# Kernel optimization log

Hardware: AMD Instinct MI355X
Metric: run time of the kernel (lower is better)

Reference implementation:

```python
import jax, jax.numpy as jnp
import numpy as np

D_MODEL = 1024
N_HEADS = 16
D_K = D_MODEL // N_HEADS
B, S = 2, 2048


def setup_inputs() -> dict:
    key = jax.random.key(0)
    ks = jax.random.split(key, 12)
    s = 1.0 / np.sqrt(D_MODEL)
    inp = {
        "query": jax.random.normal(ks[0], (B, S, D_MODEL), jnp.float32),
        "key": jax.random.normal(ks[1], (B, S, D_MODEL), jnp.float32),
        "value": jax.random.normal(ks[2], (B, S, D_MODEL), jnp.float32),
        "W_q": jax.random.uniform(ks[3], (D_MODEL, D_MODEL), jnp.float32, -s, s),
        "b_q": jnp.zeros((D_MODEL,), jnp.float32),
        "W_k": jax.random.uniform(ks[4], (D_MODEL, D_MODEL), jnp.float32, -s, s),
        "b_k": jnp.zeros((D_MODEL,), jnp.float32),
        "W_v": jax.random.uniform(ks[5], (D_MODEL, D_MODEL), jnp.float32, -s, s),
        "b_v": jnp.zeros((D_MODEL,), jnp.float32),
        "W_o": jax.random.uniform(ks[6], (D_MODEL, D_MODEL), jnp.float32, -s, s),
        "b_o": jnp.zeros((D_MODEL,), jnp.float32),
        "ln_gamma": jnp.ones((D_MODEL,), jnp.float32),
        "ln_beta": jnp.zeros((D_MODEL,), jnp.float32),
    }
    return inp


def _layer_norm(x, gamma, beta, eps=1e-5):
    mu = jnp.mean(x, axis=-1, keepdims=True)
    var = jnp.var(x, axis=-1, keepdims=True)
    return (x - mu) * jax.lax.rsqrt(var + eps) * gamma + beta


def reference(query, key, value, W_q, b_q, W_k, b_k, W_v, b_v, W_o, b_o, ln_gamma, ln_beta):
    b, s, _ = query.shape
    # projections -> [b, h, s, d_k]
    q = (query @ W_q.T + b_q).reshape(b, s, N_HEADS, D_K).transpose(0, 2, 1, 3)
    k = (key @ W_k.T + b_k).reshape(b, s, N_HEADS, D_K).transpose(0, 2, 1, 3)
    v = (value @ W_v.T + b_v).reshape(b, s, N_HEADS, D_K).transpose(0, 2, 1, 3)
    # scaled dot-product attention (no mask)
    scores = jnp.einsum('bhqd,bhkd->bhqk', q, k) / jnp.sqrt(jnp.float32(D_K))
    attn = jax.nn.softmax(scores, axis=-1)
    ctx = jnp.einsum('bhqk,bhkd->bhqd', attn, v)  # [b,h,s,d_k]
    ctx = ctx.transpose(0, 2, 1, 3).reshape(b, s, D_MODEL)
    out = ctx @ W_o.T + b_o
    # residual uses the PROJECTED query (quirk of original module); dropout=identity (eval)
    resid = q.transpose(0, 2, 1, 3).reshape(b, s, D_MODEL)
    return _layer_norm(out + resid, ln_gamma, ln_beta)
```

## Files before the change

### kernel.cpp

```cpp
#include <hip/hip_runtime.h>

#define DM 1024
#define NH 16
#define DKq 64
#define BB 2
#define SS 2048
#define MTOT 4096

#define K2f 0.18033688011112042f
#define IK2f 5.545177444479562f

typedef __attribute__((ext_vector_type(4))) float f32x4;
typedef __attribute__((ext_vector_type(16))) float f32x16;
typedef __attribute__((ext_vector_type(8))) short s16x8;
typedef __attribute__((ext_vector_type(4))) short s16x4;
typedef __attribute__((ext_vector_type(4))) unsigned short u16x4;

__device__ __forceinline__ unsigned short f2bf(float f) {
    unsigned u = __float_as_uint(f);
    u += 0x7fff + ((u >> 16) & 1);
    return (unsigned short)(u >> 16);
}

__device__ __forceinline__ float bf2f(unsigned short x) {
    return __uint_as_float((unsigned)x << 16);
}

__device__ __forceinline__ s16x8 cvt8(f32x4 a, f32x4 b) {
    s16x8 r;
    r[0] = (short)f2bf(a[0]); r[1] = (short)f2bf(a[1]);
    r[2] = (short)f2bf(a[2]); r[3] = (short)f2bf(a[3]);
    r[4] = (short)f2bf(b[0]); r[5] = (short)f2bf(b[1]);
    r[6] = (short)f2bf(b[2]); r[7] = (short)f2bf(b[3]);
    return r;
}

__device__ __forceinline__ unsigned pkp(float a, float b) {
    return __builtin_amdgcn_perm(__float_as_uint(b), __float_as_uint(a), 0x07060302u);
}

__device__ __forceinline__ void gload_lds16(const void* g, void* l) {
    __builtin_amdgcn_global_load_lds(
        (const __attribute__((address_space(1))) unsigned int*)g,
        (__attribute__((address_space(3))) unsigned int*)l,
        16, 0, 0);
}

__global__ __launch_bounds__(256)
void cvt_kernel(const float* __restrict__ s0, const float* __restrict__ s1,
                const float* __restrict__ s2, const float* __restrict__ s3,
                const float* __restrict__ s4, const float* __restrict__ s5,
                const float* __restrict__ s6,
                unsigned short* __restrict__ Xb, unsigned short* __restrict__ Wb)
{
    const int seg = blockIdx.y;
    const float* src;
    unsigned short* dst;
    int n;
    if (seg < 3) {
        src = (seg == 0) ? s0 : (seg == 1) ? s1 : s2;
        dst = Xb + (size_t)seg * (MTOT * DM);
        n = MTOT * DM;
    } else {
        src = (seg == 3) ? s3 : (seg == 4) ? s4 : (seg == 5) ? s5 : s6;
        dst = Wb + (size_t)(seg - 3) * (DM * DM);
        n = DM * DM;
    }
    const int stride = gridDim.x * 256;
    for (int i = blockIdx.x * 256 + threadIdx.x; i * 8 < n; i += stride) {
        f32x4 a = *(const f32x4*)(src + (size_t)i * 8);
        f32x4 b = *(const f32x4*)(src + (size_t)i * 8 + 4);
        *(s16x8*)(dst + (size_t)i * 8) = cvt8(a, b);
    }
}

__global__ __launch_bounds__(256, 3)
void proj_kernel(const unsigned short* __restrict__ Xb,
                 const unsigned short* __restrict__ Wb,
                 const float* __restrict__ bq, const float* __restrict__ bk,
                 const float* __restrict__ bv,
                 unsigned short* __restrict__ Qh, unsigned short* __restrict__ Kh,
                 unsigned short* __restrict__ Vt)
{
    const int bid = blockIdx.x;
    const int t   = (bid & 7) * 96 + (bid >> 3);
    const int z   = t >> 8;
    const int ty  = (t >> 3) & 31;
    const int tx  = t & 7;

    const unsigned short* X = Xb + (size_t)z * (MTOT * DM);
    const unsigned short* W = Wb + (size_t)z * (DM * DM);
    const float* bias = (z == 0) ? bq : (z == 1) ? bk : bv;

    const int m0 = ty * 128;
    const int n0 = tx * 128;
    const int tid  = threadIdx.x;
    const int lane = tid & 63;
    const int w    = tid >> 6;
    const int wm   = w >> 1, wn = w & 1;

    __shared__ __align__(16) short lA[2][128 * 32];
    __shared__ __align__(16) short lB[2][128 * 32];

    f32x4 acc[4][4];
#pragma unroll
    for (int i = 0; i < 4; i++)
#pragma unroll
        for (int j = 0; j < 4; j++) acc[i][j] = (f32x4)(0.f);

    const int srow16 = lane >> 2;
    const int scg    = lane & 3;

#define PSTAGE(BUF, KC) {                                                     \
    const int k0_ = (KC) * 32;                                                \
    _Pragma("unroll")                                                         \
    for (int p = 0; p < 2; ++p) {                                             \
        int c = w * 2 + p;                                                    \
        int row = c * 16 + srow16;                                            \
        int kc = scg ^ ((row >> 1) & 3);                                      \
        gload_lds16(X + (size_t)(m0 + row) * DM + k0_ + kc * 8,               \
                    (char*)lA[BUF] + c * 1024);                               \
        gload_lds16(W + (size_t)(n0 + row) * DM + k0_ + kc * 8,               \
                    (char*)lB[BUF] + c * 1024);                               \
    } }

#define PCOMPUTE(BUF) {                                                       \
    s16x8 af[4], bf[4];                                                       \
    const int kq = lane >> 4;                                                 \
    _Pragma("unroll")                                                         \
    for (int i = 0; i < 4; i++) {                                             \
        int row = wm * 64 + i * 16 + (lane & 15);                             \
        int slot = kq ^ ((row >> 1) & 3);                                     \
        af[i] = *(const s16x8*)((const char*)lA[BUF] + row * 64 + slot * 16); \
    }                                                                         \
    _Pragma("unroll")                                                         \
    for (int i = 0; i < 4; i++) {                                             \
        int row = wn * 64 + i * 16 + (lane & 15);                             \
        int slot = kq ^ ((row >> 1) & 3);                                     \
        bf[i] = *(const s16x8*)((const char*)lB[BUF] + row * 64 + slot * 16); \
    }                                                                         \
    _Pragma("unroll")                                                         \
    for (int i = 0; i < 4; i++)                                               \
        _Pragma("unroll")                                                     \
        for (int j = 0; j < 4; j++)                                           \
            acc[i][j] = __builtin_amdgcn_mfma_f32_16x16x32_bf16(              \
                af[i], bf[j], acc[i][j], 0, 0, 0);                            \
    }

    PSTAGE(0, 0);
    __syncthreads();
    for (int kp = 0; kp < 16; ++kp) {
        const int k2 = kp * 2;
        if (k2 + 1 < 32) PSTAGE(1, k2 + 1);
        PCOMPUTE(0);
        __syncthreads();
        if (k2 + 2 < 32) PSTAGE(0, k2 + 2);
        PCOMPUTE(1);
        __syncthreads();
    }
#undef PSTAGE
#undef PCOMPUTE

#pragma unroll
    for (int i = 0; i < 4; i++) {
#pragma unroll
        for (int j = 0; j < 4; j++) {
            int rg0 = m0 + wm * 64 + i * 16 + 4 * (lane >> 4);
            int cg  = n0 + wn * 64 + j * 16 + (lane & 15);
            int b = rg0 >> 11, s0 = rg0 & 2047, h = cg >> 6, d = cg & 63;
            float bv_ = bias[cg];
            if (z == 2) {
                int s0p = (s0 & ~12) | ((s0 & 4) << 1) | ((s0 & 8) >> 1);
                u16x4 st;
#pragma unroll
                for (int e = 0; e < 4; e++) st[e] = f2bf(acc[i][j][e] + bv_);
                *(u16x4*)&Vt[(((size_t)(b * NH + h)) * DKq + d) * SS + s0p] = st;
            } else if (z == 0) {
#pragma unroll
                for (int e = 0; e < 4; e++)
                    Qh[(((size_t)(b * NH + h)) * SS + s0 + e) * DKq + d] =
                        f2bf((acc[i][j][e] + bv_) * K2f);
            } else {
#pragma unroll
                for (int e = 0; e < 4; e++)
                    Kh[(((size_t)(b * NH + h)) * SS + s0 + e) * DKq + d] =
                        f2bf(acc[i][j][e] + bv_);
            }
        }
    }
}

__device__ __forceinline__ void attn_tile32(
    const char* __restrict__ lkc, const char* __restrict__ lvc,
    const s16x8* aq, s16x8 onesv, int l31, int hi,
    f32x16& o0, f32x16& o1, f32x16& o4)
{
    f32x16 s0 = (f32x16)(0.f), s1 = (f32x16)(0.f);
    const int sw = (l31 & 7) << 4;
    __builtin_amdgcn_s_setprio(1);
#pragma unroll
    for (int kkd = 0; kkd < 4; kkd++) {
        const int byte = (32 * kkd + 16 * hi) ^ sw;
        s16x8 ak0 = *(const s16x8*)(lkc + l31 * 128 + byte);
        s0 = __builtin_amdgcn_mfma_f32_32x32x16_bf16(ak0, aq[kkd], s0, 0, 0, 0);
        s16x8 ak1 = *(const s16x8*)(lkc + (32 + l31) * 128 + byte);
        s1 = __builtin_amdgcn_mfma_f32_32x32x16_bf16(ak1, aq[kkd], s1, 0, 0, 0);
    }
    __builtin_amdgcn_s_setprio(0);

#pragma unroll
    for (int r = 0; r < 16; r++) {
        s0[r] = __builtin_amdgcn_exp2f(s0[r]);
        s1[r] = __builtin_amdgcn_exp2f(s1[r]);
    }

    __builtin_amdgcn_s_setprio(1);
#pragma unroll
    for (int jb = 0; jb < 2; jb++) {
#pragma unroll
        for (int u = 0; u < 2; u++) {
            const int t = 2 * jb + u;
            union { unsigned uu[4]; s16x8 v; } bp;
            if (jb == 0) {
                bp.uu[0] = pkp(s0[8*u+0], s0[8*u+1]);
                bp.uu[1] = pkp(s0[8*u+2], s0[8*u+3]);
                bp.uu[2] = pkp(s0[8*u+4], s0[8*u+5]);
                bp.uu[3] = pkp(s0[8*u+6], s0[8*u+7]);
            } else {
                bp.uu[0] = pkp(s1[8*u+0], s1[8*u+1]);
                bp.uu[1] = pkp(s1[8*u+2], s1[8*u+3]);
                bp.uu[2] = pkp(s1[8*u+4], s1[8*u+5]);
                bp.uu[3] = pkp(s1[8*u+6], s1[8*u+7]);
            }
            const int vbyte = (32 * t + 16 * hi) ^ sw;
            s16x8 av0 = *(const s16x8*)(lvc + l31 * 128 + vbyte);
            o0 = __builtin_amdgcn_mfma_f32_32x32x16_bf16(av0, bp.v, o0, 0, 0, 0);
            s16x8 av1 = *(const s16x8*)(lvc + (32 + l31) * 128 + vbyte);
            o1 = __builtin_amdgcn_mfma_f32_32x32x16_bf16(av1, bp.v, o1, 0, 0, 0);
            o4 = __builtin_amdgcn_mfma_f32_32x32x16_bf16(onesv, bp.v, o4, 0, 0, 0);
        }
    }
    __builtin_amdgcn_s_setprio(0);
}

__global__ __launch_bounds__(256)
void attn_kernel(const unsigned short* __restrict__ Qh,
                 const unsigned short* __restrict__ Kh,
                 const unsigned short* __restrict__ Vt,
                 unsigned short* __restrict__ Ctx)
{
    const int bid = blockIdx.x;
    const int tt  = (bid & 7) * 64 + (bid >> 3);
    const int bh  = tt >> 4;
    const int q0  = (tt & 15) * 128;

    const int tid = threadIdx.x, lane = tid & 63, w = tid >> 6;
    const int b = bh >> 4, h = bh & 15;
    const int l31 = lane & 31;
    const int hi  = lane >> 5;

    __shared__ __align__(16) short lKs[2][64 * 64];
    __shared__ __align__(16) short lVs[2][64 * 64];

    const size_t qk_base = (size_t)bh * SS * DKq;
    const size_t vt_base = (size_t)bh * DKq * SS;

    s16x8 aq[4];
    const int qrow = q0 + 32 * w + l31;
    {
        const unsigned short* qp = Qh + qk_base + (size_t)qrow * DKq + 8 * hi;
#pragma unroll
        for (int kkd = 0; kkd < 4; kkd++)
            aq[kkd] = *(const s16x8*)(qp + 16 * kkd);
    }

    s16x8 onesv;
#pragma unroll
    for (int i = 0; i < 8; i++) onesv[i] = (short)0x3F80;

    f32x16 o0 = (f32x16)(0.f), o1 = (f32x16)(0.f), o4 = (f32x16)(0.f);

    const int lrow = lane >> 3;
    const int lcg  = (lane & 7) ^ lrow;

#define STAGE(BUF, KV0) {                                                     \
    char* dk = (char*)lKs[BUF]; char* dv = (char*)lVs[BUF];                   \
    _Pragma("unroll")                                                         \
    for (int p = 0; p < 2; ++p) {                                             \
        int c = 2 * w + p;                                                    \
        gload_lds16(Kh + qk_base + (size_t)((KV0) + c * 8 + lrow) * DKq + lcg * 8, \
                    dk + c * 1024);                                           \
        gload_lds16(Vt + vt_base + (size_t)(c * 8 + lrow) * SS + (KV0) + lcg * 8,  \
                    dv + c * 1024);                                           \
    } }

    STAGE(0, 0);
    __syncthreads();

    for (int th = 0; th < 16; ++th) {
        const int t0 = th * 2;
        STAGE(1, (t0 + 1) * 64);
        attn_tile32((const char*)lKs[0], (const char*)lVs[0], aq, onesv, l31, hi, o0, o1, o4);
        __syncthreads();
        if (t0 + 2 < 32) STAGE(0, (t0 + 2) * 64);
        attn_tile32((const char*)lKs[1], (const char*)lVs[1], aq, onesv, l31, hi, o0, o1, o4);
        __syncthreads();
    }
#undef STAGE

    const float inv = 1.0f / o4[0];
    unsigned short* crow = Ctx + ((size_t)(b * SS + qrow)) * DM + h * 64;
#pragma unroll
    for (int db = 0; db < 2; db++) {
#pragma unroll
        for (int v = 0; v < 4; v++) {
            u16x4 st;
#pragma unroll
            for (int e = 0; e < 4; e++) {
                float x = (db == 0) ? o0[4 * v + e] : o1[4 * v + e];
                st[e] = f2bf(x * inv);
            }
            *(u16x4*)(crow + 32 * db + 8 * v + 4 * hi) = st;
        }
    }
}

__global__ __launch_bounds__(256)
void outproj_kernel(const unsigned short* __restrict__ Ctx,
                    const unsigned short* __restrict__ Wo,
                    const float* __restrict__ bo,
                    const unsigned short* __restrict__ Qh,
                    float* __restrict__ Out)
{
    const int bid = blockIdx.x;
    const int t   = (bid & 7) * 32 + (bid >> 3);
    const int ty  = t >> 3;
    const int tx  = t & 7;

    const int m0 = ty * 128;
    const int n0 = tx * 128;
    const int tid = threadIdx.x, lane = tid & 63, w = tid >> 6;
    const int wm = w >> 1, wn = w & 1;

    __shared__ __align__(16) short lA[2][128 * 64];
    __shared__ __align__(16) short lB[2][128 * 64];

    f32x4 acc[4][4];
#pragma unroll
    for (int i = 0; i < 4; i++)
#pragma unroll
        for (int j = 0; j < 4; j++) acc[i][j] = (f32x4)(0.f);

    const int lrow = lane >> 3;
    const int lcg  = (lane & 7) ^ lrow;

#define PSTAGE(BUF, KT) {                                                     \
    const int k0_ = (KT) * 64;                                                \
    _Pragma("unroll")                                                         \
    for (int p = 0; p < 4; ++p) {                                             \
        int c = w * 4 + p;                                                    \
        int row = c * 8 + lrow;                                               \
        gload_lds16(Ctx + (size_t)(m0 + row) * DM + k0_ + lcg * 8,            \
                    (char*)lA[BUF] + c * 1024);                               \
        gload_lds16(Wo + (size_t)(n0 + row) * DM + k0_ + lcg * 8,             \
                    (char*)lB[BUF] + c * 1024);                               \
    } }

#define PCOMPUTE(BUF) {                                                       \
    _Pragma("unroll")                                                         \
    for (int kk = 0; kk < 2; ++kk) {                                          \
        s16x8 af[4], bf[4];                                                   \
        _Pragma("unroll")                                                     \
        for (int i = 0; i < 4; i++) {                                         \
            int row = wm * 64 + i * 16 + (lane & 15);                         \
            int byte = (kk * 64 + 16 * (lane >> 4)) ^ ((row & 7) << 4);       \
            af[i] = *(const s16x8*)((const char*)lA[BUF] + row * 128 + byte); \
        }                                                                     \
        _Pragma("unroll")                                                     \
        for (int i = 0; i < 4; i++) {                                         \
            int row = wn * 64 + i * 16 + (lane & 15);                         \
            int byte = (kk * 64 + 16 * (lane >> 4)) ^ ((row & 7) << 4);       \
            bf[i] = *(const s16x8*)((const char*)lB[BUF] + row * 128 + byte); \
        }                                                                     \
        _Pragma("unroll")                                                     \
        for (int i = 0; i < 4; i++)                                           \
            _Pragma("unroll")                                                 \
            for (int j = 0; j < 4; j++)                                       \
                acc[i][j] = __builtin_amdgcn_mfma_f32_16x16x32_bf16(          \
                    af[i], bf[j], acc[i][j], 0, 0, 0);                        \
    } }

    PSTAGE(0, 0);
    __syncthreads();
    for (int kh = 0; kh < 8; ++kh) {
        const int k0 = kh * 2;
        if (k0 + 1 < 16) PSTAGE(1, k0 + 1);
        PCOMPUTE(0);
        __syncthreads();
        if (k0 + 2 < 16) PSTAGE(0, k0 + 2);
        PCOMPUTE(1);
        __syncthreads();
    }
#undef PSTAGE
#undef PCOMPUTE

#pragma unroll
    for (int i = 0; i < 4; i++) {
#pragma unroll
        for (int j = 0; j < 4; j++) {
            int rg0 = m0 + wm * 64 + i * 16 + 4 * (lane >> 4);
            int cg  = n0 + wn * 64 + j * 16 + (lane & 15);
            int b = rg0 >> 11, s0 = rg0 & 2047, h = cg >> 6, d = cg & 63;
            float bo_ = bo[cg];
#pragma unroll
            for (int e = 0; e < 4; e++) {
                float res = bf2f(Qh[(((size_t)(b * NH + h)) * SS + s0 + e) * DKq + d]);
                Out[(size_t)(rg0 + e) * DM + cg] =
                    __builtin_fmaf(res, IK2f, acc[i][j][e] + bo_);
            }
        }
    }
}

__global__ __launch_bounds__(256)
void ln_kernel(float* __restrict__ Out, const float* __restrict__ gamma,
               const float* __restrict__ beta)
{
    const int row = blockIdx.x;
    float* rp = Out + (size_t)row * DM;
    const int tid = threadIdx.x;

    f32x4 x = *(const f32x4*)(rp + tid * 4);
    float s  = x[0] + x[1] + x[2] + x[3];
    float sq = x[0] * x[0] + x[1] * x[1] + x[2] * x[2] + x[3] * x[3];
#pragma unroll
    for (int off = 1; off < 64; off <<= 1) {
        s  += __shfl_xor(s, off);
        sq += __shfl_xor(sq, off);
    }
    __shared__ float ps[4], pq[4];
    const int w = tid >> 6;
    if ((tid & 63) == 0) { ps[w] = s; pq[w] = sq; }
    __syncthreads();
    float ts = ps[0] + ps[1] + ps[2] + ps[3];
    float tq = pq[0] + pq[1] + pq[2] + pq[3];
    float mu  = ts * (1.f / 1024.f);
    float var = tq * (1.f / 1024.f) - mu * mu;
    float rst = rsqrtf(var + 1e-5f);

    f32x4 g  = *(const f32x4*)(gamma + tid * 4);
    f32x4 bt = *(const f32x4*)(beta + tid * 4);
    f32x4 y;
#pragma unroll
    for (int e = 0; e < 4; e++) y[e] = (x[e] - mu) * rst * g[e] + bt[e];
    *(f32x4*)(rp + tid * 4) = y;
}

extern "C" void kernel_launch(void* const* d_in, const int* in_sizes, int n_in,
                              void* d_out, int out_size, void* d_ws, size_t ws_size,
                              hipStream_t stream)
{
    const float* query = (const float*)d_in[0];
    const float* key   = (const float*)d_in[1];
    const float* value = (const float*)d_in[2];
    const float* Wq = (const float*)d_in[3];
    const float* bq = (const float*)d_in[4];
    const float* Wk = (const float*)d_in[5];
    const float* bk = (const float*)d_in[6];
    const float* Wv = (const float*)d_in[7];
    const float* bv = (const float*)d_in[8];
    const float* Wo = (const float*)d_in[9];
    const float* bo = (const float*)d_in[10];
    const float* gamma = (const float*)d_in[11];
    const float* beta  = (const float*)d_in[12];

    char* ws = (char*)d_ws;
    unsigned short* Xb  = (unsigned short*)(ws);
    unsigned short* Wb  = (unsigned short*)(ws + (24u << 20));
    unsigned short* Qh  = (unsigned short*)(ws + (32u << 20));
    unsigned short* Kh  = (unsigned short*)(ws + (40u << 20));
    unsigned short* Vt  = (unsigned short*)(ws + (48u << 20));
    unsigned short* Ctx = (unsigned short*)(ws);
    float* Out = (float*)d_out;

    cvt_kernel<<<dim3(256, 7), 256, 0, stream>>>(query, key, value,
                                                 Wq, Wk, Wv, Wo, Xb, Wb);
    proj_kernel<<<768, 256, 0, stream>>>(Xb, Wb, bq, bk, bv, Qh, Kh, Vt);
    attn_kernel<<<512, 256, 0, stream>>>(Qh, Kh, Vt, Ctx);
    outproj_kernel<<<256, 256, 0, stream>>>(Ctx, Wb + 3u * DM * DM, bo, Qh, Out);
    ln_kernel<<<4096, 256, 0, stream>>>(Out, gamma, beta);
}
```

Baseline: 132.3 us.

## Process 64 query rows per wave in attention and drop ones-MFMA row sum

Each attention wave now handles two 32-row query sub-tiles, so every K and V fragment read from LDS feeds two MFMAs instead of one. Blocks shrink from 4 to 2 waves, and each wave stages twice as many K/V chunks. The softmax denominator is now summed in scalar registers after exp2, with a cross-half shuffle at the end, instead of a separate ones-vector MFMA. This cuts LDS traffic and MFMA count, but roughly doubles accumulator register use, which may reduce occupancy and leaves fewer waves per block to hide latency.

```diff
diff --git a/kernel.cpp b/kernel.cpp
--- a/kernel.cpp
+++ b/kernel.cpp
@@ -190,29 +190,41 @@
     }
 }
 
-__device__ __forceinline__ void attn_tile32(
+__device__ __forceinline__ void attn_tile64(
     const char* __restrict__ lkc, const char* __restrict__ lvc,
-    const s16x8* aq, s16x8 onesv, int l31, int hi,
-    f32x16& o0, f32x16& o1, f32x16& o4)
-{
-    f32x16 s0 = (f32x16)(0.f), s1 = (f32x16)(0.f);
+    const s16x8* aqa, const s16x8* aqb, int l31, int hi,
+    f32x16& o0a, f32x16& o1a, f32x16& o0b, f32x16& o1b,
+    float& rsa, float& rsb)
+{
+    f32x16 s0a = (f32x16)(0.f), s1a = (f32x16)(0.f);
+    f32x16 s0b = (f32x16)(0.f), s1b = (f32x16)(0.f);
     const int sw = (l31 & 7) << 4;
     __builtin_amdgcn_s_setprio(1);
 #pragma unroll
     for (int kkd = 0; kkd < 4; kkd++) {
         const int byte = (32 * kkd + 16 * hi) ^ sw;
         s16x8 ak0 = *(const s16x8*)(lkc + l31 * 128 + byte);
-        s0 = __builtin_amdgcn_mfma_f32_32x32x16_bf16(ak0, aq[kkd], s0, 0, 0, 0);
+        s0a = __builtin_amdgcn_mfma_f32_32x32x16_bf16(ak0, aqa[kkd], s0a, 0, 0, 0);
+        s0b = __builtin_amdgcn_mfma_f32_32x32x16_bf16(ak0, aqb[kkd], s0b, 0, 0, 0);
         s16x8 ak1 = *(const s16x8*)(lkc + (32 + l31) * 128 + byte);
-        s1 = __builtin_amdgcn_mfma_f32_32x32x16_bf16(ak1, aq[kkd], s1, 0, 0, 0);
+        s1a = __builtin_amdgcn_mfma_f32_32x32x16_bf16(ak1, aqa[kkd], s1a, 0, 0, 0);
+        s1b = __builtin_amdgcn_mfma_f32_32x32x16_bf16(ak1, aqb[kkd], s1b, 0, 0, 0);
     }
     __builtin_amdgcn_s_setprio(0);
 
+    float ra = 0.f, rb = 0.f;
 #pragma unroll
     for (int r = 0; r < 16; r++) {
-        s0[r] = __builtin_amdgcn_exp2f(s0[r]);
-        s1[r] = __builtin_amdgcn_exp2f(s1[r]);
-    }
+        float a0 = __builtin_amdgcn_exp2f(s0a[r]);
+        float a1 = __builtin_amdgcn_exp2f(s1a[r]);
+        float b0 = __builtin_amdgcn_exp2f(s0b[r]);
+        float b1 = __builtin_amdgcn_exp2f(s1b[r]);
+        s0a[r] = a0; s1a[r] = a1; s0b[r] = b0; s1b[r] = b1;
+        ra += a0 + a1;
+        rb += b0 + b1;
+    }
+    rsa += ra;
+    rsb += rb;
 
     __builtin_amdgcn_s_setprio(1);
 #pragma unroll
@@ -220,30 +232,39 @@
 #pragma unroll
         for (int u = 0; u < 2; u++) {
             const int t = 2 * jb + u;
-            union { unsigned uu[4]; s16x8 v; } bp;
+            union { unsigned uu[4]; s16x8 v; } bpa, bpb;
             if (jb == 0) {
-                bp.uu[0] = pkp(s0[8*u+0], s0[8*u+1]);
-                bp.uu[1] = pkp(s0[8*u+2], s0[8*u+3]);
-                bp.uu[2] = pkp(s0[8*u+4], s0[8*u+5]);
-                bp.uu[3] = pkp(s0[8*u+6], s0[8*u+7]);
+                bpa.uu[0] = pkp(s0a[8*u+0], s0a[8*u+1]);
+                bpa.uu[1] = pkp(s0a[8*u+2], s0a[8*u+3]);
+                bpa.uu[2] = pkp(s0a[8*u+4], s0a[8*u+5]);
+                bpa.uu[3] = pkp(s0a[8*u+6], s0a[8*u+7]);
+                bpb.uu[0] = pkp(s0b[8*u+0], s0b[8*u+1]);
+                bpb.uu[1] = pkp(s0b[8*u+2], s0b[8*u+3]);
+                bpb.uu[2] = pkp(s0b[8*u+4], s0b[8*u+5]);
+                bpb.uu[3] = pkp(s0b[8*u+6], s0b[8*u+7]);
             } else {
-                bp.uu[0] = pkp(s1[8*u+0], s1[8*u+1]);
-                bp.uu[1] = pkp(s1[8*u+2], s1[8*u+3]);
-                bp.uu[2] = pkp(s1[8*u+4], s1[8*u+5]);
-                bp.uu[3] = pkp(s1[8*u+6], s1[8*u+7]);
+                bpa.uu[0] = pkp(s1a[8*u+0], s1a[8*u+1]);
+                bpa.uu[1] = pkp(s1a[8*u+2], s1a[8*u+3]);
+                bpa.uu[2] = pkp(s1a[8*u+4], s1a[8*u+5]);
+                bpa.uu[3] = pkp(s1a[8*u+6], s1a[8*u+7]);
+                bpb.uu[0] = pkp(s1b[8*u+0], s1b[8*u+1]);
+                bpb.uu[1] = pkp(s1b[8*u+2], s1b[8*u+3]);
+                bpb.uu[2] = pkp(s1b[8*u+4], s1b[8*u+5]);
+                bpb.uu[3] = pkp(s1b[8*u+6], s1b[8*u+7]);
             }
             const int vbyte = (32 * t + 16 * hi) ^ sw;
             s16x8 av0 = *(const s16x8*)(lvc + l31 * 128 + vbyte);
-            o0 = __builtin_amdgcn_mfma_f32_32x32x16_bf16(av0, bp.v, o0, 0, 0, 0);
+            o0a = __builtin_amdgcn_mfma_f32_32x32x16_bf16(av0, bpa.v, o0a, 0, 0, 0);
+            o0b = __builtin_amdgcn_mfma_f32_32x32x16_bf16(av0, bpb.v, o0b, 0, 0, 0);
             s16x8 av1 = *(const s16x8*)(lvc + (32 + l31) * 128 + vbyte);
-            o1 = __builtin_amdgcn_mfma_f32_32x32x16_bf16(av1, bp.v, o1, 0, 0, 0);
-            o4 = __builtin_amdgcn_mfma_f32_32x32x16_bf16(onesv, bp.v, o4, 0, 0, 0);
+            o1a = __builtin_amdgcn_mfma_f32_32x32x16_bf16(av1, bpa.v, o1a, 0, 0, 0);
+            o1b = __builtin_amdgcn_mfma_f32_32x32x16_bf16(av1, bpb.v, o1b, 0, 0, 0);
         }
     }
     __builtin_amdgcn_s_setprio(0);
 }
 
-__global__ __launch_bounds__(256)
+__global__ __launch_bounds__(128, 2)
 void attn_kernel(const unsigned short* __restrict__ Qh,
                  const unsigned short* __restrict__ Kh,
                  const unsigned short* __restrict__ Vt,
@@ -265,20 +286,22 @@
     const size_t qk_base = (size_t)bh * SS * DKq;
     const size_t vt_base = (size_t)bh * DKq * SS;
 
-    s16x8 aq[4];
-    const int qrow = q0 + 32 * w + l31;
+    s16x8 aqa[4], aqb[4];
+    const int qa = q0 + 64 * w + l31;
+    const int qb = qa + 32;
     {
-        const unsigned short* qp = Qh + qk_base + (size_t)qrow * DKq + 8 * hi;
-#pragma unroll
-        for (int kkd = 0; kkd < 4; kkd++)
-            aq[kkd] = *(const s16x8*)(qp + 16 * kkd);
-    }
-
-    s16x8 onesv;
-#pragma unroll
-    for (int i = 0; i < 8; i++) onesv[i] = (short)0x3F80;
-
-    f32x16 o0 = (f32x16)(0.f), o1 = (f32x16)(0.f), o4 = (f32x16)(0.f);
+        const unsigned short* qpa = Qh + qk_base + (size_t)qa * DKq + 8 * hi;
+        const unsigned short* qpb = Qh + qk_base + (size_t)qb * DKq + 8 * hi;
+#pragma unroll
+        for (int kkd = 0; kkd < 4; kkd++) {
+            aqa[kkd] = *(const s16x8*)(qpa + 16 * kkd);
+            aqb[kkd] = *(const s16x8*)(qpb + 16 * kkd);
+        }
+    }
+
+    f32x16 o0a = (f32x16)(0.f), o1a = (f32x16)(0.f);
+    f32x16 o0b = (f32x16)(0.f), o1b = (f32x16)(0.f);
+    float rsa = 0.f, rsb = 0.f;
 
     const int lrow = lane >> 3;
     const int lcg  = (lane & 7) ^ lrow;
@@ -286,8 +309,8 @@
 #define STAGE(BUF, KV0) {                                                     \
     char* dk = (char*)lKs[BUF]; char* dv = (char*)lVs[BUF];                   \
     _Pragma("unroll")                                                         \
-    for (int p = 0; p < 2; ++p) {                                             \
-        int c = 2 * w + p;                                                    \
+    for (int p = 0; p < 4; ++p) {                                             \
+        int c = 4 * w + p;                                                    \
         gload_lds16(Kh + qk_base + (size_t)((KV0) + c * 8 + lrow) * DKq + lcg * 8, \
                     dk + c * 1024);                                           \
         gload_lds16(Vt + vt_base + (size_t)(c * 8 + lrow) * SS + (KV0) + lcg * 8,  \
@@ -300,27 +323,36 @@
     for (int th = 0; th < 16; ++th) {
         const int t0 = th * 2;
         STAGE(1, (t0 + 1) * 64);
-        attn_tile32((const char*)lKs[0], (const char*)lVs[0], aq, onesv, l31, hi, o0, o1, o4);
+        attn_tile64((const char*)lKs[0], (const char*)lVs[0], aqa, aqb, l31, hi,
+                    o0a, o1a, o0b, o1b, rsa, rsb);
         __syncthreads();
         if (t0 + 2 < 32) STAGE(0, (t0 + 2) * 64);
-        attn_tile32((const char*)lKs[1], (const char*)lVs[1], aq, onesv, l31, hi, o0, o1, o4);
+        attn_tile64((const char*)lKs[1], (const char*)lVs[1], aqa, aqb, l31, hi,
+                    o0a, o1a, o0b, o1b, rsa, rsb);
         __syncthreads();
     }
 #undef STAGE
 
-    const float inv = 1.0f / o4[0];
-    unsigned short* crow = Ctx + ((size_t)(b * SS + qrow)) * DM + h * 64;
+    rsa += __shfl_xor(rsa, 32);
+    rsb += __shfl_xor(rsb, 32);
+    const float inva = 1.0f / rsa;
+    const float invb = 1.0f / rsb;
+    unsigned short* crowa = Ctx + ((size_t)(b * SS + qa)) * DM + h * 64;
+    unsigned short* crowb = Ctx + ((size_t)(b * SS + qb)) * DM + h * 64;
 #pragma unroll
     for (int db = 0; db < 2; db++) {
 #pragma unroll
         for (int v = 0; v < 4; v++) {
-            u16x4 st;
+            u16x4 sta, stb;
 #pragma unroll
             for (int e = 0; e < 4; e++) {
-                float x = (db == 0) ? o0[4 * v + e] : o1[4 * v + e];
-                st[e] = f2bf(x * inv);
+                float xa = (db == 0) ? o0a[4 * v + e] : o1a[4 * v + e];
+                float xb = (db == 0) ? o0b[4 * v + e] : o1b[4 * v + e];
+                sta[e] = f2bf(xa * inva);
+                stb[e] = f2bf(xb * invb);
             }
-            *(u16x4*)(crow + 32 * db + 8 * v + 4 * hi) = st;
+            *(u16x4*)(crowa + 32 * db + 8 * v + 4 * hi) = sta;
+            *(u16x4*)(crowb + 32 * db + 8 * v + 4 * hi) = stb;
         }
     }
 }
@@ -486,7 +518,7 @@
     cvt_kernel<<<dim3(256, 7), 256, 0, stream>>>(query, key, value,
                                                  Wq, Wk, Wv, Wo, Xb, Wb);
     proj_kernel<<<768, 256, 0, stream>>>(Xb, Wb, bq, bk, bv, Qh, Kh, Vt);
-    attn_kernel<<<512, 256, 0, stream>>>(Qh, Kh, Vt, Ctx);
+    attn_kernel<<<512, 128, 0, stream>>>(Qh, Kh, Vt, Ctx);
     outproj_kernel<<<256, 256, 0, stream>>>(Ctx, Wb + 3u * DM * DM, bo, Qh, Out);
     ln_kernel<<<4096, 256, 0, stream>>>(Out, gamma, beta);
 }
```

Result: slower. 143.0 us (+8.1%).
